# Optimization experiments

Measured on AMD Instinct MI355X. Metric: run time of the kernel, lower is better.

## Reference

```python
import jax, jax.numpy as jnp
import numpy as np

EPS = 1e-6


def rms_norm(h, w):
    # T5-style: no mean subtraction, no bias; variance in fp32
    var = jnp.mean(jnp.square(h.astype(jnp.float32)), axis=-1, keepdims=True)
    h = h * jax.lax.rsqrt(var + EPS)
    return w * h


def split_heads(t, n_heads):
    b, n, d = t.shape
    return t.reshape(b, n, n_heads, d // n_heads).transpose(0, 2, 1, 3)  # [B,H,N,dk]


def unify_heads(t):
    b, h, n, dk = t.shape
    return t.transpose(0, 2, 1, 3).reshape(b, n, h * dk)


def attention(q_in, kv_in, bias, wq, wk, wv, wo, n_heads):
    q = split_heads(q_in @ wq, n_heads)   # [B,H,Nq,dk]
    k = split_heads(kv_in @ wk, n_heads)  # [B,H,Nk,dk]
    v = split_heads(kv_in @ wv, n_heads)
    scores = jnp.einsum('bhqd,bhkd->bhqk', q, k) + bias  # no 1/sqrt(dk) scaling (T5 style)
    w = jax.nn.softmax(scores.astype(jnp.float32), axis=-1).astype(scores.dtype)
    out = jnp.einsum('bhqk,bhkd->bhqd', w, v)
    return unify_heads(out) @ wo


def setup_inputs() -> dict:
    key = jax.random.key(0)
    ks = jax.random.split(key, 18)
    B, N, ENC_N, D, H, DFF = 4, 2048, 1024, 1024, 16, 4096
    s = 0.02
    inp = {
        'x': jax.random.normal(ks[0], (B, N, D), jnp.float32),
        'encoding': jax.random.normal(ks[1], (B, ENC_N, D), jnp.float32),
        'self_attention_position_bias': jax.random.normal(ks[2], (1, H, 1, N), jnp.float32),
        'enc_dec_attention_position_bias': jax.random.normal(ks[3], (1, H, N, ENC_N), jnp.float32),
        'wq_s': jax.random.normal(ks[4], (D, D), jnp.float32) * s,
        'wk_s': jax.random.normal(ks[5], (D, D), jnp.float32) * s,
        'wv_s': jax.random.normal(ks[6], (D, D), jnp.float32) * s,
        'wo_s': jax.random.normal(ks[7], (D, D), jnp.float32) * s,
        'wq_c': jax.random.normal(ks[8], (D, D), jnp.float32) * s,
        'wk_c': jax.random.normal(ks[9], (D, D), jnp.float32) * s,
        'wv_c': jax.random.normal(ks[10], (D, D), jnp.float32) * s,
        'wo_c': jax.random.normal(ks[11], (D, D), jnp.float32) * s,
        'ff1_w': jax.random.normal(ks[12], (D, DFF), jnp.float32) * s,
        'ff2_w': jax.random.normal(ks[13], (DFF, D), jnp.float32) * s,
        'norm1_w': jnp.ones((D,), jnp.float32),
        'norm2_w': jnp.ones((D,), jnp.float32),
        'norm3_w': jnp.ones((D,), jnp.float32),
    }
    return inp


def reference(x, encoding, self_attention_position_bias, enc_dec_attention_position_bias,
              wq_s, wk_s, wv_s, wo_s, wq_c, wk_c, wv_c, wo_c,
              ff1_w, ff2_w, norm1_w, norm2_w, norm3_w):
    n_heads = 16
    # --- self-attention (decoder: single query = last token) ---
    normed = rms_norm(x, norm1_w)
    q_in = normed[:, -1:, :]  # [B,1,D]
    attn_out = attention(q_in, normed, self_attention_position_bias,
                         wq_s, wk_s, wv_s, wo_s, n_heads)  # [B,1,D]
    x = x + attn_out  # broadcast over sequence, matching torch in-place broadcast
    # --- cross-attention ---
    normed = rms_norm(x, norm2_w)
    cross_out = attention(normed, encoding, enc_dec_attention_position_bias,
                          wq_c, wk_c, wv_c, wo_c, n_heads)  # [B,N,D]
    x = x + cross_out
    # --- MLP ---
    normed = rms_norm(x, norm3_w)
    mlp_out = jax.nn.relu(normed @ ff1_w) @ ff2_w
    return x + mlp_out
```

## Files before the change

kernel.cpp:

```cpp
#include <hip/hip_runtime.h>
#include <stdint.h>

typedef unsigned short bfu;
typedef __bf16 bf8v __attribute__((ext_vector_type(8)));
typedef unsigned short us8 __attribute__((ext_vector_type(8)));
typedef unsigned short us4 __attribute__((ext_vector_type(4)));
typedef float f4v __attribute__((ext_vector_type(4)));

__device__ __forceinline__ float bf2f(bfu u) {
    union { unsigned u; float f; } c; c.u = ((unsigned)u) << 16; return c.f;
}
__device__ __forceinline__ bfu f2bf(float f) {
    union { float f; unsigned u; } c; c.f = f;
    unsigned r = c.u + 0x7fffu + ((c.u >> 16) & 1u);
    return (bfu)(r >> 16);
}
__device__ __forceinline__ f4v mfma16(us8 a, us8 b, f4v c) {
    return __builtin_amdgcn_mfma_f32_16x16x32_bf16(
        __builtin_bit_cast(bf8v, a), __builtin_bit_cast(bf8v, b), c, 0, 0, 0);
}

template<int BM, int BN, int EPI>
__global__ __launch_bounds__(256) void gemm_bt(
    const bfu* __restrict__ A, const bfu* __restrict__ Bt,
    const float* __restrict__ resF, void* __restrict__ outP,
    int K, int lda, int ldb, int ldc,
    long long aZs, long long aBs, long long aHs,
    long long bZs, long long bBs, long long bHs,
    long long cZs, long long cBs, long long cHs,
    int bh0)
{
    constexpr int BK = 64;
    constexpr int WM = BM / 2, WN = BN / 2;
    constexpr int TM = WM / 16, TN = WN / 16;
    __shared__ __align__(16) bfu sA[BM * BK];
    __shared__ __align__(16) bfu sB[BN * BK];

    const int tid  = threadIdx.x;
    const int lane = tid & 63;
    const int wid  = tid >> 6;
    const int wr = wid >> 1, wc = wid & 1;

    const int z  = blockIdx.z;
    const int bh = bh0 + z;
    const int bb = bh >> 4, hh = bh & 15;
    const long long aOff = aZs * z + aBs * bb + aHs * hh;
    const long long bOff = bZs * z + bBs * bb + bHs * hh;
    const long long cOff = cZs * z + cBs * bb + cHs * hh;

    const int m0 = blockIdx.y * BM;
    const int n0 = blockIdx.x * BN;

    f4v acc[TM][TN];
    #pragma unroll
    for (int i = 0; i < TM; ++i)
        #pragma unroll
        for (int j = 0; j < TN; ++j)
            acc[i][j] = (f4v)0.0f;

    const bfu* gA = A + aOff + (long long)m0 * lda;
    const bfu* gB = Bt + bOff + (long long)n0 * ldb;
    const int rsub = tid >> 3;
    const int kb   = (tid & 7) * 8;

    for (int k0 = 0; k0 < K; k0 += BK) {
        us8 ra[BM / 32], rb[BN / 32];
        #pragma unroll
        for (int it = 0; it < BM / 32; ++it)
            ra[it] = *(const us8*)(gA + (long long)(it * 32 + rsub) * lda + k0 + kb);
        #pragma unroll
        for (int it = 0; it < BN / 32; ++it)
            rb[it] = *(const us8*)(gB + (long long)(it * 32 + rsub) * ldb + k0 + kb);

        __syncthreads();
        #pragma unroll
        for (int it = 0; it < BM / 32; ++it)
            *(us8*)&sA[(it * 32 + rsub) * BK + kb] = ra[it];
        #pragma unroll
        for (int it = 0; it < BN / 32; ++it)
            *(us8*)&sB[(it * 32 + rsub) * BK + kb] = rb[it];
        __syncthreads();

        #pragma unroll
        for (int kk = 0; kk < BK; kk += 32) {
            const int kro = kk + ((lane >> 4) << 3);
            us8 af[TM], bfr[TN];
            #pragma unroll
            for (int i = 0; i < TM; ++i)
                af[i] = *(const us8*)&sA[(wr * WM + i * 16 + (lane & 15)) * BK + kro];
            #pragma unroll
            for (int j = 0; j < TN; ++j)
                bfr[j] = *(const us8*)&sB[(wc * WN + j * 16 + (lane & 15)) * BK + kro];
            #pragma unroll
            for (int i = 0; i < TM; ++i)
                #pragma unroll
                for (int j = 0; j < TN; ++j)
                    acc[i][j] = mfma16(af[i], bfr[j], acc[i][j]);
        }
    }

    const int quad = lane >> 4;
    const int cn = lane & 15;
    #pragma unroll
    for (int i = 0; i < TM; ++i) {
        #pragma unroll
        for (int j = 0; j < TN; ++j) {
            const int col = n0 + wc * WN + j * 16 + cn;
            #pragma unroll
            for (int r = 0; r < 4; ++r) {
                const int row = m0 + wr * WM + i * 16 + quad * 4 + r;
                const long long idx = cOff + (long long)row * ldc + col;
                const float v = acc[i][j][r];
                if constexpr (EPI == 0) ((bfu*)outP)[idx] = f2bf(v);
                else if constexpr (EPI == 1) ((float*)outP)[idx] = resF[idx] + v;
                else ((bfu*)outP)[idx] = f2bf(fmaxf(v, 0.0f));
            }
        }
    }
}

#define SROW 1036
__global__ __launch_bounds__(256, 4) void xattn(
    const bfu* __restrict__ q2,
    const bfu* __restrict__ k2,
    const bfu* __restrict__ v2t,
    const float* __restrict__ bias,
    bfu* __restrict__ O)
{
    __shared__ __align__(16) bfu S[16 * SROW];
    const int tid = threadIdx.x, lane = tid & 63, wid = tid >> 6;
    const int quad = lane >> 4, l16 = lane & 15;
    const int bh = blockIdx.y, b = bh >> 4, h = bh & 15;
    const int q0 = blockIdx.x * 16;

    const int kh0 = wid * 256;
    const bfu* qbase = q2 + ((long long)b * 2048 + q0) * 1024 + h * 64;
    const us8 af0 = *(const us8*)(qbase + (long long)l16 * 1024 + quad * 8);
    const us8 af1 = *(const us8*)(qbase + (long long)l16 * 1024 + 32 + quad * 8);
    const bfu* kbase = k2 + (long long)b * 1048576 + h * 64;
    #pragma unroll 4
    for (int t = 0; t < 16; ++t) {
        const int n0 = kh0 + t * 16;
        const bfu* kr = kbase + (long long)(n0 + l16) * 1024 + quad * 8;
        const us8 bf0 = *(const us8*)kr;
        const us8 bf1 = *(const us8*)(kr + 32);
        f4v acc = (f4v)0.0f;
        acc = mfma16(af0, bf0, acc);
        acc = mfma16(af1, bf1, acc);
        #pragma unroll
        for (int r = 0; r < 4; ++r)
            S[(quad * 4 + r) * SROW + n0 + l16] = f2bf(acc[r]);
    }
    __syncthreads();

    const float* bb0 = bias + ((long long)h * 2048 + q0) * 1024;
    #pragma unroll 2
    for (int rr = 0; rr < 4; ++rr) {
        const int row = wid * 4 + rr;
        bfu* sp = &S[row * SROW + lane * 16];
        const us8 s0 = *(const us8*)sp;
        const us8 s1 = *(const us8*)(sp + 8);
        const float* bp = bb0 + (long long)row * 1024 + lane * 16;
        f4v bv[4];
        #pragma unroll
        for (int j = 0; j < 4; ++j) bv[j] = *(const f4v*)(bp + j * 4);
        float v[16];
        #pragma unroll
        for (int j = 0; j < 8; ++j) v[j] = bf2f(s0[j]) + bv[j >> 2][j & 3];
        #pragma unroll
        for (int j = 0; j < 8; ++j) v[8 + j] = bf2f(s1[j]) + bv[2 + (j >> 2)][j & 3];
        float m = v[0];
        #pragma unroll
        for (int j = 1; j < 16; ++j) m = fmaxf(m, v[j]);
        #pragma unroll
        for (int o = 32; o; o >>= 1) m = fmaxf(m, __shfl_xor(m, o));
        float s = 0.f;
        #pragma unroll
        for (int j = 0; j < 16; ++j) { v[j] = __expf(v[j] - m); s += v[j]; }
        #pragma unroll
        for (int o = 32; o; o >>= 1) s += __shfl_xor(s, o);
        const float inv = 1.0f / s;
        us8 o0, o1;
        #pragma unroll
        for (int j = 0; j < 8; ++j) { o0[j] = f2bf(v[j] * inv); o1[j] = f2bf(v[8 + j] * inv); }
        *(us8*)sp = o0;
        *(us8*)(sp + 8) = o1;
    }
    __syncthreads();

    const bfu* vb = v2t + (long long)bh * 65536 + (long long)(wid * 16 + l16) * 1024;
    f4v acc3 = (f4v)0.0f;
    #pragma unroll 4
    for (int k0 = 0; k0 < 1024; k0 += 32) {
        const us8 pa = *(const us8*)&S[l16 * SROW + k0 + quad * 8];
        const us8 vf = *(const us8*)(vb + k0 + quad * 8);
        acc3 = mfma16(pa, vf, acc3);
    }
    bfu* ob = O + ((long long)b * 2048 + q0) * 1024 + h * 64 + wid * 16;
    #pragma unroll
    for (int r = 0; r < 4; ++r)
        ob[(long long)(quad * 4 + r) * 1024 + l16] = f2bf(acc3[r]);
}

__global__ __launch_bounds__(256) void cvt_f2b(
    const float* __restrict__ in, bfu* __restrict__ out)
{
    const long long i = ((long long)blockIdx.x * 256 + threadIdx.x) * 4;
    f4v v = *(const f4v*)(in + i);
    us4 o;
    #pragma unroll
    for (int k = 0; k < 4; ++k) o[k] = f2bf(v[k]);
    *(us4*)(out + i) = o;
}

__global__ __launch_bounds__(256) void transpose_plain(
    const float* __restrict__ in, bfu* __restrict__ out, int R, int C)
{
    __shared__ bfu t[32][33];
    const int r0 = blockIdx.y * 32, c0 = blockIdx.x * 32;
    const int tx = threadIdx.x, ty = threadIdx.y;
    #pragma unroll
    for (int i = 0; i < 32; i += 8)
        t[ty + i][tx] = f2bf(in[(long long)(r0 + ty + i) * C + c0 + tx]);
    __syncthreads();
    #pragma unroll
    for (int i = 0; i < 32; i += 8)
        out[(long long)(c0 + ty + i) * R + r0 + tx] = t[tx][ty + i];
}

__global__ __launch_bounds__(256) void transpose_w8(
    const float* p0, const float* p1, const float* p2, const float* p3,
    const float* p4, const float* p5, const float* p6, const float* p7,
    bfu* __restrict__ out)
{
    __shared__ bfu t[32][33];
    const float* srcs[8] = {p0, p1, p2, p3, p4, p5, p6, p7};
    const int zz = blockIdx.z;
    const float* in = srcs[zz];
    bfu* o = out + (long long)zz * 1048576;
    const int r0 = blockIdx.y * 32, c0 = blockIdx.x * 32;
    const int tx = threadIdx.x, ty = threadIdx.y;
    #pragma unroll
    for (int i = 0; i < 32; i += 8)
        t[ty + i][tx] = f2bf(in[(long long)(r0 + ty + i) * 1024 + c0 + tx]);
    __syncthreads();
    #pragma unroll
    for (int i = 0; i < 32; i += 8)
        o[(long long)(c0 + ty + i) * 1024 + r0 + tx] = t[tx][ty + i];
}

__global__ __launch_bounds__(256) void transpose_v2(
    const bfu* __restrict__ v2, bfu* __restrict__ v2t)
{
    __shared__ bfu t[32][33];
    const int z = blockIdx.z, b = z >> 4, h = z & 15;
    const bfu* in = v2 + (long long)b * 1048576 + h * 64;
    bfu* o = v2t + (long long)z * 65536;
    const int c0 = blockIdx.x * 32, r0 = blockIdx.y * 32;
    const int tx = threadIdx.x, ty = threadIdx.y;
    #pragma unroll
    for (int i = 0; i < 32; i += 8)
        t[ty + i][tx] = in[(long long)(r0 + ty + i) * 1024 + c0 + tx];
    __syncthreads();
    #pragma unroll
    for (int i = 0; i < 32; i += 8)
        o[(long long)(c0 + ty + i) * 1024 + r0 + tx] = t[tx][ty + i];
}

__device__ __forceinline__ float blockSum4(float v, float* red) {
    const int lane = threadIdx.x & 63, wid = threadIdx.x >> 6;
    #pragma unroll
    for (int o = 32; o; o >>= 1) v += __shfl_xor(v, o);
    if (lane == 0) red[wid] = v;
    __syncthreads();
    return red[0] + red[1] + red[2] + red[3];
}

__global__ __launch_bounds__(256) void rmsnorm_f32k(
    const float* __restrict__ X, const float* __restrict__ w, bfu* __restrict__ O)
{
    __shared__ float red[4];
    const long long row = blockIdx.x;
    const int tid = threadIdx.x;
    f4v xv = *(const f4v*)(X + row * 1024 + tid * 4);
    float ss = 0.f;
    #pragma unroll
    for (int i = 0; i < 4; ++i) ss += xv[i] * xv[i];
    ss = blockSum4(ss, red);
    const float sc = rsqrtf(ss * (1.0f / 1024.0f) + 1e-6f);
    f4v wv = *(const f4v*)(w + tid * 4);
    us4 o4;
    #pragma unroll
    for (int i = 0; i < 4; ++i) o4[i] = f2bf(xv[i] * sc * wv[i]);
    *(us4*)(O + row * 1024 + tid * 4) = o4;
}

__global__ __launch_bounds__(256) void add_bcast_rmsnorm(
    const float* __restrict__ X, const float* __restrict__ attn,
    const float* __restrict__ w, float* __restrict__ X1, bfu* __restrict__ O)
{
    __shared__ float red[4];
    const long long row = blockIdx.x;
    const int b = (int)(row >> 11);
    const int tid = threadIdx.x;
    f4v xv = *(const f4v*)(X + row * 1024 + tid * 4);
    f4v av = *(const f4v*)(attn + b * 1024 + tid * 4);
    f4v v;
    float ss = 0.f;
    #pragma unroll
    for (int i = 0; i < 4; ++i) { v[i] = xv[i] + av[i]; ss += v[i] * v[i]; }
    *(f4v*)(X1 + row * 1024 + tid * 4) = v;
    ss = blockSum4(ss, red);
    const float sc = rsqrtf(ss * (1.0f / 1024.0f) + 1e-6f);
    f4v wv = *(const f4v*)(w + tid * 4);
    us4 o4;
    #pragma unroll
    for (int i = 0; i < 4; ++i) o4[i] = f2bf(v[i] * sc * wv[i]);
    *(us4*)(O + row * 1024 + tid * 4) = o4;
}

template<int OUTF>
__global__ __launch_bounds__(256) void vecmat(
    const bfu* __restrict__ A, const bfu* __restrict__ Bt, void* __restrict__ out,
    int K, int N, long long aStride, long long aBase)
{
    __shared__ float sa[1024];
    const int tid = threadIdx.x;
    const int b = blockIdx.y;
    const bfu* ar = A + aBase + (long long)b * aStride;
    for (int k = tid; k < K; k += 256) sa[k] = bf2f(ar[k]);
    __syncthreads();
    const int n = blockIdx.x * 256 + tid;
    if (n < N) {
        const bfu* wr = Bt + (long long)n * K;
        float s = 0.f;
        for (int k = 0; k < K; k += 8) {
            us8 wv = *(const us8*)(wr + k);
            #pragma unroll
            for (int j = 0; j < 8; ++j) s += sa[k + j] * bf2f(wv[j]);
        }
        if constexpr (OUTF) ((float*)out)[(long long)b * N + n] = s;
        else ((bfu*)out)[(long long)b * N + n] = f2bf(s);
    }
}

__global__ __launch_bounds__(256) void decode_attn(
    const bfu* __restrict__ qs, const bfu* __restrict__ Kt,
    const bfu* __restrict__ Vt, const float* __restrict__ bias,
    bfu* __restrict__ osmall)
{
    const int bh = blockIdx.x, b = bh >> 4, h = bh & 15;
    const int tid = threadIdx.x, lane = tid & 63, wid = tid >> 6;
    __shared__ float sq[64];
    __shared__ float sc[2048];
    __shared__ float red[4];
    __shared__ float po[4][64];
    if (tid < 64) sq[tid] = bf2f(qs[b * 1024 + h * 64 + tid]);
    __syncthreads();

    const bfu* Kb = Kt + (long long)b * 2048 * 1024 + h * 64;
    float lmax = -1e30f;
    for (int k = tid; k < 2048; k += 256) {
        const us8* kr = (const us8*)(Kb + (long long)k * 1024);
        float s = 0.f;
        #pragma unroll
        for (int j = 0; j < 8; ++j) {
            us8 kv = kr[j];
            #pragma unroll
            for (int t = 0; t < 8; ++t) s += sq[j * 8 + t] * bf2f(kv[t]);
        }
        s += bias[h * 2048 + k];
        sc[k] = s;
        lmax = fmaxf(lmax, s);
    }
    #pragma unroll
    for (int o = 32; o; o >>= 1) lmax = fmaxf(lmax, __shfl_xor(lmax, o));
    if (lane == 0) red[wid] = lmax;
    __syncthreads();
    const float m = fmaxf(fmaxf(red[0], red[1]), fmaxf(red[2], red[3]));
    __syncthreads();

    float lsum = 0.f;
    for (int k = tid; k < 2048; k += 256) {
        const float e = __expf(sc[k] - m);
        sc[k] = e; lsum += e;
    }
    #pragma unroll
    for (int o = 32; o; o >>= 1) lsum += __shfl_xor(lsum, o);
    if (lane == 0) red[wid] = lsum;
    __syncthreads();
    const float S = red[0] + red[1] + red[2] + red[3];

    const bfu* Vb = Vt + (long long)b * 2048 * 1024 + h * 64;
    const int d = tid & 63, ks = tid >> 6;
    float a = 0.f;
    for (int k = ks * 512; k < ks * 512 + 512; ++k)
        a += sc[k] * bf2f(Vb[(long long)k * 1024 + d]);
    po[ks][d] = a;
    __syncthreads();
    if (tid < 64) {
        const float r = (po[0][tid] + po[1][tid] + po[2][tid] + po[3][tid]) / S;
        osmall[b * 1024 + h * 64 + tid] = f2bf(r);
    }
}

extern "C" void kernel_launch(void* const* d_in, const int* in_sizes, int n_in,
                              void* d_out, int out_size, void* d_ws, size_t ws_size,
                              hipStream_t stream) {
    (void)in_sizes; (void)n_in; (void)out_size; (void)ws_size;
    const float* x     = (const float*)d_in[0];
    const float* enc   = (const float*)d_in[1];
    const float* sbias = (const float*)d_in[2];
    const float* cbias = (const float*)d_in[3];
    const float* wq_s  = (const float*)d_in[4];
    const float* wk_s  = (const float*)d_in[5];
    const float* wv_s  = (const float*)d_in[6];
    const float* wo_s  = (const float*)d_in[7];
    const float* wq_c  = (const float*)d_in[8];
    const float* wk_c  = (const float*)d_in[9];
    const float* wv_c  = (const float*)d_in[10];
    const float* wo_c  = (const float*)d_in[11];
    const float* ff1   = (const float*)d_in[12];
    const float* ff2   = (const float*)d_in[13];
    const float* n1w   = (const float*)d_in[14];
    const float* n2w   = (const float*)d_in[15];
    const float* n3w   = (const float*)d_in[16];
    float* out = (float*)d_out;

    char* ws = (char*)d_ws;
    size_t off = 0;
    auto alloc = [&](size_t bytes) -> void* {
        void* p = (void*)(ws + off);
        off += (bytes + 255) & ~(size_t)255;
        return p;
    };
    bfu*   normed = (bfu*)alloc((size_t)8192 * 1024 * 2);
    bfu*   bufA   = (bfu*)alloc((size_t)8192 * 1024 * 2);
    bfu*   bufB   = (bfu*)alloc((size_t)8192 * 1024 * 2);
    bfu*   k2b    = (bfu*)alloc((size_t)4096 * 1024 * 2);
    bfu*   v2b    = (bfu*)alloc((size_t)4096 * 1024 * 2);
    bfu*   v2t    = (bfu*)alloc((size_t)4096 * 1024 * 2);
    bfu*   encb   = (bfu*)alloc((size_t)4096 * 1024 * 2);
    float* x1f    = (float*)alloc((size_t)8192 * 1024 * 4);
    bfu*   wT     = (bfu*)alloc((size_t)8 * 1048576 * 2);
    bfu*   ff1T   = (bfu*)alloc((size_t)4096 * 1024 * 2);
    bfu*   ff2T   = (bfu*)alloc((size_t)4096 * 1024 * 2);
    bfu*   qsb    = (bfu*)alloc(4 * 1024 * 2);
    bfu*   osm    = (bfu*)alloc(4 * 1024 * 2);
    float* attnv  = (float*)alloc(4 * 1024 * 4);
    bfu*   H1     = bufA;

    const dim3 tb32(32, 8);

    cvt_f2b<<<dim3(4096), 256, 0, stream>>>(enc, encb);
    transpose_w8<<<dim3(32, 32, 8), tb32, 0, stream>>>(
        wq_s, wk_s, wv_s, wo_s, wq_c, wk_c, wv_c, wo_c, wT);
    transpose_plain<<<dim3(128, 32, 1), tb32, 0, stream>>>(ff1, ff1T, 1024, 4096);
    transpose_plain<<<dim3(32, 128, 1), tb32, 0, stream>>>(ff2, ff2T, 4096, 1024);

    rmsnorm_f32k<<<dim3(8192), 256, 0, stream>>>(x, n1w, normed);

    gemm_bt<128, 128, 0><<<dim3(8, 64, 1), 256, 0, stream>>>(
        normed, wT + 1 * 1048576, nullptr, bufA, 1024, 1024, 1024, 1024,
        0, 0, 0, 0, 0, 0, 0, 0, 0, 0);
    gemm_bt<128, 128, 0><<<dim3(8, 64, 1), 256, 0, stream>>>(
        normed, wT + 2 * 1048576, nullptr, bufB, 1024, 1024, 1024, 1024,
        0, 0, 0, 0, 0, 0, 0, 0, 0, 0);
    vecmat<0><<<dim3(4, 4), 256, 0, stream>>>(normed, wT + 0 * 1048576, qsb,
        1024, 1024, (long long)2048 * 1024, (long long)2047 * 1024);
    decode_attn<<<dim3(64), 256, 0, stream>>>(qsb, bufA, bufB, sbias, osm);
    vecmat<1><<<dim3(4, 4), 256, 0, stream>>>(osm, wT + 3 * 1048576, attnv,
        1024, 1024, 1024, 0);
    add_bcast_rmsnorm<<<dim3(8192), 256, 0, stream>>>(x, attnv, n2w, x1f, normed);

    gemm_bt<128, 128, 0><<<dim3(8, 64, 1), 256, 0, stream>>>(
        normed, wT + 4 * 1048576, nullptr, bufA, 1024, 1024, 1024, 1024,
        0, 0, 0, 0, 0, 0, 0, 0, 0, 0);
    gemm_bt<128, 128, 0><<<dim3(8, 32, 1), 256, 0, stream>>>(
        encb, wT + 5 * 1048576, nullptr, k2b, 1024, 1024, 1024, 1024,
        0, 0, 0, 0, 0, 0, 0, 0, 0, 0);
    gemm_bt<128, 128, 0><<<dim3(8, 32, 1), 256, 0, stream>>>(
        encb, wT + 6 * 1048576, nullptr, v2b, 1024, 1024, 1024, 1024,
        0, 0, 0, 0, 0, 0, 0, 0, 0, 0);
    transpose_v2<<<dim3(2, 32, 64), tb32, 0, stream>>>(v2b, v2t);

    xattn<<<dim3(128, 64), 256, 0, stream>>>(bufA, k2b, v2t, cbias, bufB);

    gemm_bt<128, 128, 1><<<dim3(8, 64, 1), 256, 0, stream>>>(
        bufB, wT + 7 * 1048576, x1f, x1f, 1024, 1024, 1024, 1024,
        0, 0, 0, 0, 0, 0, 0, 0, 0, 0);

    rmsnorm_f32k<<<dim3(8192), 256, 0, stream>>>(x1f, n3w, normed);
    for (int mc = 0; mc < 8192; mc += 4096) {
        gemm_bt<128, 128, 2><<<dim3(32, 32, 1), 256, 0, stream>>>(
            normed + (long long)mc * 1024, ff1T, nullptr, H1,
            1024, 1024, 1024, 4096,
            0, 0, 0, 0, 0, 0, 0, 0, 0, 0);
        gemm_bt<128, 128, 1><<<dim3(8, 32, 1), 256, 0, stream>>>(
            H1, ff2T, x1f + (long long)mc * 1024, out + (long long)mc * 1024,
            4096, 4096, 4096, 1024,
            0, 0, 0, 0, 0, 0, 0, 0, 0, 0);
    }
}
```

Baseline: 1.113 ms.

## Use direct global-to-LDS loads in GEMM and prefetch bias in cross-attention

The GEMM tile loop now uses global_load_lds to copy A/B tiles straight into shared memory, skipping the register staging. The cross-attention kernel issues its bias loads early so they overlap the QK^T phase, and remaps blockIdx.y so the four batches sharing a head's bias run adjacent, which should improve L2 reuse. The P·V loop is batched into 8 loads per step with two independent accumulators to expose more memory- and MFMA-level parallelism. The GEMM change drops the overlap between the next tile's global load and the current tile's compute, and raises register pressure in the attention kernel.

```diff
diff --git a/kernel.cpp b/kernel.cpp
--- a/kernel.cpp
+++ b/kernel.cpp
@@ -18,6 +18,11 @@
 __device__ __forceinline__ f4v mfma16(us8 a, us8 b, f4v c) {
     return __builtin_amdgcn_mfma_f32_16x16x32_bf16(
         __builtin_bit_cast(bf8v, a), __builtin_bit_cast(bf8v, b), c, 0, 0, 0);
+}
+__device__ __forceinline__ void gll16(const bfu* g, bfu* l) {
+    __builtin_amdgcn_global_load_lds(
+        (const __attribute__((address_space(1))) void*)g,
+        (__attribute__((address_space(3))) void*)l, 16, 0, 0);
 }
 
 template<int BM, int BN, int EPI>
@@ -64,21 +69,15 @@
     const int kb   = (tid & 7) * 8;
 
     for (int k0 = 0; k0 < K; k0 += BK) {
-        us8 ra[BM / 32], rb[BN / 32];
+        __syncthreads();
         #pragma unroll
         for (int it = 0; it < BM / 32; ++it)
-            ra[it] = *(const us8*)(gA + (long long)(it * 32 + rsub) * lda + k0 + kb);
+            gll16(gA + (long long)(it * 32 + rsub) * lda + k0 + kb,
+                  &sA[(it * 32 + rsub) * BK + kb]);
         #pragma unroll
         for (int it = 0; it < BN / 32; ++it)
-            rb[it] = *(const us8*)(gB + (long long)(it * 32 + rsub) * ldb + k0 + kb);
-
-        __syncthreads();
-        #pragma unroll
-        for (int it = 0; it < BM / 32; ++it)
-            *(us8*)&sA[(it * 32 + rsub) * BK + kb] = ra[it];
-        #pragma unroll
-        for (int it = 0; it < BN / 32; ++it)
-            *(us8*)&sB[(it * 32 + rsub) * BK + kb] = rb[it];
+            gll16(gB + (long long)(it * 32 + rsub) * ldb + k0 + kb,
+                  &sB[(it * 32 + rsub) * BK + kb]);
         __syncthreads();
 
         #pragma unroll
@@ -130,8 +129,18 @@
     __shared__ __align__(16) bfu S[16 * SROW];
     const int tid = threadIdx.x, lane = tid & 63, wid = tid >> 6;
     const int quad = lane >> 4, l16 = lane & 15;
-    const int bh = blockIdx.y, b = bh >> 4, h = bh & 15;
+    const int yb = blockIdx.y;
+    const int b = yb & 3, h = yb >> 2;
+    const int bhv = b * 16 + h;
     const int q0 = blockIdx.x * 16;
+
+    const float* bp = bias + ((long long)h * 2048 + q0 + wid * 4) * 1024 + lane * 16;
+    f4v bv01[2][4];
+    #pragma unroll
+    for (int rr = 0; rr < 2; ++rr)
+        #pragma unroll
+        for (int j = 0; j < 4; ++j)
+            bv01[rr][j] = *(const f4v*)(bp + (long long)rr * 1024 + j * 4);
 
     const int kh0 = wid * 256;
     const bfu* qbase = q2 + ((long long)b * 2048 + q0) * 1024 + h * 64;
@@ -151,19 +160,21 @@
         for (int r = 0; r < 4; ++r)
             S[(quad * 4 + r) * SROW + n0 + l16] = f2bf(acc[r]);
     }
-    __syncthreads();
-
-    const float* bb0 = bias + ((long long)h * 2048 + q0) * 1024;
+    f4v bv23[2][4];
+    #pragma unroll
+    for (int rr = 0; rr < 2; ++rr)
+        #pragma unroll
+        for (int j = 0; j < 4; ++j)
+            bv23[rr][j] = *(const f4v*)(bp + (long long)(2 + rr) * 1024 + j * 4);
+    __syncthreads();
+
     #pragma unroll 2
     for (int rr = 0; rr < 4; ++rr) {
         const int row = wid * 4 + rr;
         bfu* sp = &S[row * SROW + lane * 16];
         const us8 s0 = *(const us8*)sp;
         const us8 s1 = *(const us8*)(sp + 8);
-        const float* bp = bb0 + (long long)row * 1024 + lane * 16;
-        f4v bv[4];
-        #pragma unroll
-        for (int j = 0; j < 4; ++j) bv[j] = *(const f4v*)(bp + j * 4);
+        const f4v* bv = (rr < 2) ? bv01[rr] : bv23[rr - 2];
         float v[16];
         #pragma unroll
         for (int j = 0; j < 8; ++j) v[j] = bf2f(s0[j]) + bv[j >> 2][j & 3];
@@ -188,14 +199,22 @@
     }
     __syncthreads();
 
-    const bfu* vb = v2t + (long long)bh * 65536 + (long long)(wid * 16 + l16) * 1024;
-    f4v acc3 = (f4v)0.0f;
-    #pragma unroll 4
-    for (int k0 = 0; k0 < 1024; k0 += 32) {
-        const us8 pa = *(const us8*)&S[l16 * SROW + k0 + quad * 8];
-        const us8 vf = *(const us8*)(vb + k0 + quad * 8);
-        acc3 = mfma16(pa, vf, acc3);
-    }
+    const bfu* vb = v2t + (long long)bhv * 65536 + (long long)(wid * 16 + l16) * 1024;
+    f4v a0 = (f4v)0.0f, a1 = (f4v)0.0f;
+    for (int k0 = 0; k0 < 1024; k0 += 256) {
+        us8 pa[8], vf[8];
+        #pragma unroll
+        for (int j = 0; j < 8; ++j) {
+            pa[j] = *(const us8*)&S[l16 * SROW + k0 + j * 32 + quad * 8];
+            vf[j] = *(const us8*)(vb + k0 + j * 32 + quad * 8);
+        }
+        #pragma unroll
+        for (int j = 0; j < 8; j += 2) {
+            a0 = mfma16(pa[j],     vf[j],     a0);
+            a1 = mfma16(pa[j + 1], vf[j + 1], a1);
+        }
+    }
+    const f4v acc3 = a0 + a1;
     bfu* ob = O + ((long long)b * 2048 + q0) * 1024 + h * 64 + wid * 16;
     #pragma unroll
     for (int r = 0; r < 4; ++r)
```

Result: slower. 1.253 ms (+12.6%).
